# Performance work log

Measured on AMD Instinct MI355X. Metric: run time of the kernel, lower is better.

The kernel has to match this reference:

```python
import jax, jax.numpy as jnp
import numpy as np
import math

B, S, D, H = 16, 1024, 512, 8
DK = D // H  # 64
EPS_T = 1e-06   # temperature epsilon
LN_EPS = 1e-05  # torch LayerNorm default


def gelu_tanh(x):
    return 0.5 * x * (1 + jnp.tanh(math.sqrt(2.0 / math.pi) * (x + 0.044715 * x ** 3)))


def layer_norm(x, g, b):
    mu = jnp.mean(x, axis=-1, keepdims=True)
    var = jnp.mean((x - mu) ** 2, axis=-1, keepdims=True)
    return (x - mu) * jax.lax.rsqrt(var + LN_EPS) * g + b


def setup_inputs() -> dict:
    key = jax.random.key(0)
    ks = jax.random.split(key, 12)
    std_qkv = np.sqrt(2.0 / (D + D)).astype(np.float32)
    inp = {
        "Q": jax.random.normal(ks[0], (B, S, D), jnp.float32),
        "K": jax.random.normal(ks[1], (B, S, D), jnp.float32),
        "V": jax.random.normal(ks[2], (B, S, D), jnp.float32),
        "mask": jnp.zeros((B, S), dtype=bool),  # no padding
        "W_q": jax.random.normal(ks[3], (D, D), jnp.float32) * std_qkv,
        "W_k": jax.random.normal(ks[4], (D, D), jnp.float32) * std_qkv,
        "W_v": jax.random.normal(ks[5], (D, D), jnp.float32) * std_qkv,
        "W_o": jax.random.normal(ks[6], (D, D), jnp.float32) * std_qkv,
        "lin1_w": jax.random.normal(ks[7], (D, D), jnp.float32) * std_qkv,  # stored [in,out]
        "lin1_b": jnp.zeros((D,), jnp.float32),
        "lin2_w": jax.random.normal(ks[8], (D, D), jnp.float32) * std_qkv,
        "lin2_b": jnp.zeros((D,), jnp.float32),
        "ln_g": jnp.ones((D,), jnp.float32),
        "ln_b": jnp.zeros((D,), jnp.float32),
    }
    return inp


def reference(Q, K, V, mask, W_q, W_k, W_v, W_o, lin1_w, lin1_b, lin2_w, lin2_b, ln_g, ln_b):
    b, q_len, _ = Q.shape
    # projections -> (b, h, s, d_k)
    Qh = (Q @ W_q).reshape(b, q_len, H, DK).transpose(0, 2, 1, 3)
    Kh = (K @ W_k).reshape(b, q_len, H, DK).transpose(0, 2, 1, 3)
    Vh = (V @ W_v).reshape(b, q_len, H, DK).transpose(0, 2, 1, 3)

    temperature = DK ** 0.5
    scores = jnp.einsum("bhqd,bhkd->bhqk", Qh, Kh) / (temperature + EPS_T)

    # mask: causal triu(diag=1) OR pad mask broadcast along k (as in original)
    causal = jnp.triu(jnp.ones((q_len, q_len), dtype=bool), k=1)  # (q,k)
    pad = mask[:, None, :, None]                                  # (b,1,q,1)
    mask_ = causal[None, None, :, :] | pad                        # (b,1,q,k)
    scores = jnp.where(mask_, -1e10, scores)

    attn = jax.nn.softmax(scores, axis=-1)
    ctx = jnp.einsum("bhqk,bhkd->bhqd", attn, Vh)
    ctx = ctx.transpose(0, 2, 1, 3).reshape(b, q_len, H * DK)
    v_att = ctx @ W_o  # dropout = identity (eval)

    out = layer_norm(Q + v_att, ln_g, ln_b)
    ffn = gelu_tanh(out @ lin1_w + lin1_b) @ lin2_w + lin2_b
    out = layer_norm(ffn + out, ln_g, ln_b)
    return out
```

## Files before the change

### kernel.cpp

```cpp
#include <hip/hip_runtime.h>
#include <cstdint>

using f32x4  = __attribute__((ext_vector_type(4))) float;
using f16x8  = __attribute__((ext_vector_type(8))) _Float16;
using f16x4  = __attribute__((ext_vector_type(4))) _Float16;

#define DEV static __device__ __forceinline__

DEV _Float16 f2h(float f) { return (_Float16)f; }

DEV void gl2lds16(const void* g, void* l) {
  __builtin_amdgcn_global_load_lds(
      (__attribute__((address_space(1))) void*)(uintptr_t)g,
      (__attribute__((address_space(3))) void*)(uint32_t)(uintptr_t)l,
      16, 0, 0);
}

template <int MODE>
__global__ __launch_bounds__(256, 2) void gemm_k(
    const _Float16* __restrict__ A, const _Float16* __restrict__ Bt,
    const float* __restrict__ bias, float* __restrict__ outF,
    _Float16* __restrict__ outB) {
  __shared__ _Float16 As[128 * 32];
  __shared__ _Float16 Bs[128 * 32];
  const int tid = threadIdx.x;
  const int lane = tid & 63, wv = tid >> 6;
  const int quad = lane >> 4, l16 = lane & 15;
  const int wm = wv & 1, wn = wv >> 1;
  const int m0 = blockIdx.y * 128, n0 = blockIdx.x * 128;

  f32x4 acc[4][4] = {};

  const int c0 = tid, c1 = tid + 256;
  const int r0 = c0 >> 2, kp0 = c0 & 3, kl0 = kp0 ^ ((r0 >> 1) & 3);
  const int r1 = c1 >> 2, kp1 = c1 & 3, kl1 = kp1 ^ ((r1 >> 1) & 3);

  const _Float16* Ab = A + (size_t)m0 * 512;
  const _Float16* Bb = Bt + (size_t)n0 * 512;

  for (int kt = 0; kt < 512; kt += 32) {
    gl2lds16(Ab + (size_t)r0 * 512 + kt + kl0 * 8, &As[c0 * 8]);
    gl2lds16(Ab + (size_t)r1 * 512 + kt + kl1 * 8, &As[c1 * 8]);
    gl2lds16(Bb + (size_t)r0 * 512 + kt + kl0 * 8, &Bs[c0 * 8]);
    gl2lds16(Bb + (size_t)r1 * 512 + kt + kl1 * 8, &Bs[c1 * 8]);
    __syncthreads();
    f16x8 af[4], bfr[4];
#pragma unroll
    for (int i = 0; i < 4; i++) {
      int row = wm * 64 + i * 16 + l16;
      int q = quad ^ ((row >> 1) & 3);
      af[i] = *(const f16x8*)&As[row * 32 + q * 8];
    }
#pragma unroll
    for (int j = 0; j < 4; j++) {
      int row = wn * 64 + j * 16 + l16;
      int q = quad ^ ((row >> 1) & 3);
      bfr[j] = *(const f16x8*)&Bs[row * 32 + q * 8];
    }
#pragma unroll
    for (int i = 0; i < 4; i++)
#pragma unroll
      for (int j = 0; j < 4; j++)
        acc[i][j] = __builtin_amdgcn_mfma_f32_16x16x32_f16(af[i], bfr[j],
                                                           acc[i][j], 0, 0, 0);
    __syncthreads();
  }

#pragma unroll
  for (int i = 0; i < 4; i++) {
#pragma unroll
    for (int j = 0; j < 4; j++) {
      const size_t col = n0 + wn * 64 + j * 16 + l16;
#pragma unroll
      for (int r = 0; r < 4; r++) {
        const size_t row = m0 + wm * 64 + i * 16 + quad * 4 + r;
        float v = acc[i][j][r];
        if (MODE == 0) {
          size_t b = row >> 10, s = row & 1023, h = col >> 6, d = col & 63;
          outB[(((b * 8 + h) << 10) + s) * 64 + d] = f2h(v);
        } else if (MODE == 1) {
          outF[row * 512 + col] = v;
        } else if (MODE == 2) {
          float x = v + bias[col];
          float u = 0.7978845608028654f * (x + 0.044715f * x * x * x);
          float t = __expf(2.f * u);
          float th = 1.f - 2.f / (t + 1.f);
          outB[row * 512 + col] = f2h(0.5f * x * (1.f + th));
        } else {
          outF[row * 512 + col] = v + bias[col];
        }
      }
    }
  }
}

__global__ __launch_bounds__(256, 2) void attn_k(
    const _Float16* __restrict__ Qh, const _Float16* __restrict__ Kh,
    const _Float16* __restrict__ Vt, _Float16* __restrict__ ctx) {
  __shared__ _Float16 lds[16384];

  const int bid = blockIdx.x;
  const int qblk = 7 - (bid >> 7);
  const int bh = bid & 127;
  const int q0 = qblk * 128;
  const int ktmax = 2 * qblk + 1;

  const _Float16* Qp = Qh + (size_t)bh * 65536;
  const _Float16* Kp = Kh + (size_t)bh * 65536;
  const _Float16* Vp = Vt + (size_t)bh * 65536;

  const int tid = threadIdx.x, lane = tid & 63, wv = tid >> 6;
  const int quad = lane >> 4, l16 = lane & 15;
  const int s7 = l16 & 7;
  const int wdiag = 2 * qblk + (wv >> 1);

  f16x8 bq[2][2];
#pragma unroll
  for (int qs = 0; qs < 2; qs++)
#pragma unroll
    for (int kc = 0; kc < 2; kc++)
      bq[qs][kc] = *(const f16x8*)&Qp[(size_t)(q0 + wv * 32 + qs * 16 + l16) *
                                          64 +
                                      kc * 32 + quad * 8];
  int qg[2];
  qg[0] = q0 + wv * 32 + l16;
  qg[1] = qg[0] + 16;

  const float scale = 1.0f / (8.0f + 1e-6f);
  f32x4 ot[4][2] = {};
  float mrun[2] = {-3.0e38f, -3.0e38f};
  float lrun[2] = {0.f, 0.f};

  const int i0 = 2 * wv, i1 = 2 * wv + 1;
  const int lin0 = i0 * 64 + lane, lin1 = i1 * 64 + lane;
  const int rK0 = lin0 >> 3, chK0 = (lane & 7) ^ (rK0 & 7);
  const int rK1 = lin1 >> 3, chK1 = (lane & 7) ^ (rK1 & 7);

  auto stage = [&](int kt, int pb) {
    _Float16* Kb = lds + pb * 4096;
    _Float16* Vb = lds + 8192 + pb * 4096;
    gl2lds16(Kp + (size_t)(kt * 64 + rK0) * 64 + chK0 * 8, Kb + lin0 * 8);
    gl2lds16(Kp + (size_t)(kt * 64 + rK1) * 64 + chK1 * 8, Kb + lin1 * 8);
    gl2lds16(Vp + (size_t)rK0 * 1024 + kt * 64 + chK0 * 8, Vb + lin0 * 8);
    gl2lds16(Vp + (size_t)rK1 * 1024 + kt * 64 + chK1 * 8, Vb + lin1 * 8);
  };

  stage(0, 0);
  __syncthreads();

  for (int kt = 0; kt <= ktmax; kt++) {
    if (kt < ktmax) stage(kt + 1, (kt + 1) & 1);

    if (kt <= wdiag) {
      const _Float16* Ks = lds + (kt & 1) * 4096;
      const _Float16* Vs = lds + 8192 + (kt & 1) * 4096;

      f32x4 sa[4][2] = {};
#pragma unroll
      for (int ms = 0; ms < 4; ms++) {
        const int row = ms * 16 + l16;
        const int sl0 = quad ^ s7;
        f16x8 ka0 = *(const f16x8*)&Ks[row * 64 + sl0 * 8];
        f16x8 ka1 = *(const f16x8*)&Ks[row * 64 + (sl0 ^ 4) * 8];
#pragma unroll
        for (int qs = 0; qs < 2; qs++) {
          sa[ms][qs] = __builtin_amdgcn_mfma_f32_16x16x32_f16(
              ka0, bq[qs][0], sa[ms][qs], 0, 0, 0);
          sa[ms][qs] = __builtin_amdgcn_mfma_f32_16x16x32_f16(
              ka1, bq[qs][1], sa[ms][qs], 0, 0, 0);
        }
      }

      const bool diag = (kt == wdiag);
      float tmax[2] = {-3.0e38f, -3.0e38f};
#pragma unroll
      for (int ms = 0; ms < 4; ms++)
#pragma unroll
        for (int qs = 0; qs < 2; qs++)
#pragma unroll
          for (int r = 0; r < 4; r++) {
            float s = sa[ms][qs][r] * scale;
            if (diag) {
              int kg = kt * 64 + ms * 16 + quad * 4 + r;
              if (kg > qg[qs]) s = -3.0e38f;
            }
            sa[ms][qs][r] = s;
            tmax[qs] = fmaxf(tmax[qs], s);
          }

      float al[2];
#pragma unroll
      for (int qs = 0; qs < 2; qs++) {
        tmax[qs] = fmaxf(tmax[qs], __shfl_xor(tmax[qs], 16, 64));
        tmax[qs] = fmaxf(tmax[qs], __shfl_xor(tmax[qs], 32, 64));
        float mn = fmaxf(mrun[qs], tmax[qs]);
        al[qs] = __expf(mrun[qs] - mn);
        mrun[qs] = mn;
        lrun[qs] *= al[qs];
      }

      f16x4 pf[4][2];
#pragma unroll
      for (int ms = 0; ms < 4; ms++)
#pragma unroll
        for (int qs = 0; qs < 2; qs++) {
          f16x4 pk;
#pragma unroll
          for (int r = 0; r < 4; r++) {
            float p = __expf(sa[ms][qs][r] - mrun[qs]);
            lrun[qs] += p;
            pk[r] = f2h(p);
          }
          pf[ms][qs] = pk;
        }

#pragma unroll
      for (int ds = 0; ds < 4; ds++)
#pragma unroll
        for (int qs = 0; qs < 2; qs++)
#pragma unroll
          for (int r = 0; r < 4; r++) ot[ds][qs][r] *= al[qs];

#pragma unroll
      for (int ms = 0; ms < 4; ms++) {
        const int ch0 = (ms * 2 + (quad >> 1)) ^ s7;
#pragma unroll
        for (int ds = 0; ds < 4; ds++) {
          const int row = ds * 16 + l16;
          f16x4 vf =
              *(const f16x4*)&Vs[row * 64 + ch0 * 8 + (quad & 1) * 4];
#pragma unroll
          for (int qs = 0; qs < 2; qs++)
            ot[ds][qs] = __builtin_amdgcn_mfma_f32_16x16x16f16(
                vf, pf[ms][qs], ot[ds][qs], 0, 0, 0);
        }
      }
    }
    __syncthreads();
  }

  float rinv[2];
#pragma unroll
  for (int qs = 0; qs < 2; qs++) {
    lrun[qs] += __shfl_xor(lrun[qs], 16, 64);
    lrun[qs] += __shfl_xor(lrun[qs], 32, 64);
    rinv[qs] = 1.0f / lrun[qs];
  }

  _Float16* Ol = lds + wv * 2176;
#pragma unroll
  for (int ds = 0; ds < 4; ds++)
#pragma unroll
    for (int qs = 0; qs < 2; qs++) {
      f16x4 pk;
#pragma unroll
      for (int r = 0; r < 4; r++) pk[r] = f2h(ot[ds][qs][r] * rinv[qs]);
      *(f16x4*)&Ol[(qs * 16 + l16) * 68 + ds * 16 + quad * 4] = pk;
    }
  __syncthreads();

  const int b = bh >> 3, h = bh & 7;
#pragma unroll
  for (int rep = 0; rep < 4; rep++) {
    const int qq = rep * 8 + (lane >> 3);
    const int dc = lane & 7;
    f16x4 a = *(const f16x4*)&Ol[qq * 68 + dc * 8];
    f16x4 c = *(const f16x4*)&Ol[qq * 68 + dc * 8 + 4];
    f16x8 v;
    v[0] = a[0]; v[1] = a[1]; v[2] = a[2]; v[3] = a[3];
    v[4] = c[0]; v[5] = c[1]; v[6] = c[2]; v[7] = c[3];
    size_t row = (size_t)b * 1024 + q0 + wv * 32 + qq;
    *(f16x8*)&ctx[row * 512 + h * 64 + dc * 8] = v;
  }
}

__global__ void cast3_k(const float* __restrict__ Q, const float* __restrict__ K,
                        const float* __restrict__ V, _Float16* __restrict__ Qb,
                        _Float16* __restrict__ Kb, _Float16* __restrict__ Vb) {
  size_t i = (size_t)blockIdx.x * 256 + threadIdx.x;
  float4 q = ((const float4*)Q)[i];
  float4 k = ((const float4*)K)[i];
  float4 v = ((const float4*)V)[i];
  f16x4 o;
  o[0] = f2h(q.x); o[1] = f2h(q.y); o[2] = f2h(q.z); o[3] = f2h(q.w);
  ((f16x4*)Qb)[i] = o;
  o[0] = f2h(k.x); o[1] = f2h(k.y); o[2] = f2h(k.z); o[3] = f2h(k.w);
  ((f16x4*)Kb)[i] = o;
  o[0] = f2h(v.x); o[1] = f2h(v.y); o[2] = f2h(v.z); o[3] = f2h(v.w);
  ((f16x4*)Vb)[i] = o;
}

__global__ void wtrans_k(const float* W0, const float* W1, const float* W2,
                         const float* W3, const float* W4, const float* W5,
                         _Float16* dst) {
  __shared__ float t[32][33];
  const int z = blockIdx.z;
  const float* src = (z == 0) ? W0 : (z == 1) ? W1 : (z == 2) ? W2
                    : (z == 3) ? W3 : (z == 4) ? W4 : W5;
  _Float16* out = dst + (size_t)z * 262144;
  const int k0 = blockIdx.x * 32, n0 = blockIdx.y * 32;
  const int x = threadIdx.x, y = threadIdx.y;
  for (int j = y; j < 32; j += 8) t[j][x] = src[(size_t)(k0 + j) * 512 + n0 + x];
  __syncthreads();
  for (int j = y; j < 32; j += 8)
    out[(size_t)(n0 + j) * 512 + k0 + x] = f2h(t[x][j]);
}

__global__ void vtrans_k(const _Float16* __restrict__ Vh,
                         _Float16* __restrict__ Vt) {
  __shared__ _Float16 t[32][33];
  const int bh = blockIdx.z;
  const int s0 = blockIdx.x * 32, d0 = blockIdx.y * 32;
  const _Float16* src = Vh + (size_t)bh * 65536;
  _Float16* dst = Vt + (size_t)bh * 65536;
  const int x = threadIdx.x, y = threadIdx.y;
  for (int j = y; j < 32; j += 8) t[j][x] = src[(size_t)(s0 + j) * 64 + d0 + x];
  __syncthreads();
  for (int j = y; j < 32; j += 8)
    dst[(size_t)(d0 + j) * 1024 + s0 + x] = t[x][j];
}

template <bool WB>
__global__ __launch_bounds__(128) void ln_k(
    const float* __restrict__ X0, const float* __restrict__ X1,
    const float* __restrict__ g, const float* __restrict__ bb,
    float* __restrict__ outF, _Float16* __restrict__ outB) {
  __shared__ float sh[4];
  const int row = blockIdx.x, t = threadIdx.x;
  const size_t base = (size_t)row * 512 + t * 4;
  float4 a = *(const float4*)(X0 + base);
  float4 c = *(const float4*)(X1 + base);
  float x0 = a.x + c.x, x1 = a.y + c.y, x2 = a.z + c.z, x3 = a.w + c.w;
  float s = x0 + x1 + x2 + x3;
  float ss = x0 * x0 + x1 * x1 + x2 * x2 + x3 * x3;
#pragma unroll
  for (int off = 1; off <= 32; off <<= 1) {
    s += __shfl_xor(s, off, 64);
    ss += __shfl_xor(ss, off, 64);
  }
  if ((t & 63) == 0) { sh[(t >> 6) * 2] = s; sh[(t >> 6) * 2 + 1] = ss; }
  __syncthreads();
  s = sh[0] + sh[2];
  ss = sh[1] + sh[3];
  const float mu = s * (1.f / 512.f);
  const float var = ss * (1.f / 512.f) - mu * mu;
  const float rstd = rsqrtf(var + 1e-5f);
  float4 gv = *(const float4*)(g + t * 4);
  float4 bv = *(const float4*)(bb + t * 4);
  float y0 = (x0 - mu) * rstd * gv.x + bv.x;
  float y1 = (x1 - mu) * rstd * gv.y + bv.y;
  float y2 = (x2 - mu) * rstd * gv.z + bv.z;
  float y3 = (x3 - mu) * rstd * gv.w + bv.w;
  float4 o; o.x = y0; o.y = y1; o.z = y2; o.w = y3;
  *(float4*)(outF + base) = o;
  if (WB) {
    f16x4 ob; ob[0] = f2h(y0); ob[1] = f2h(y1); ob[2] = f2h(y2); ob[3] = f2h(y3);
    *(f16x4*)(outB + base) = ob;
  }
}

extern "C" void kernel_launch(void* const* d_in, const int* in_sizes, int n_in,
                              void* d_out, int out_size, void* d_ws,
                              size_t ws_size, hipStream_t stream) {
  const float* Q = (const float*)d_in[0];
  const float* K = (const float*)d_in[1];
  const float* V = (const float*)d_in[2];
  const float* Wq = (const float*)d_in[4];
  const float* Wk = (const float*)d_in[5];
  const float* Wv = (const float*)d_in[6];
  const float* Wo = (const float*)d_in[7];
  const float* l1w = (const float*)d_in[8];
  const float* l1b = (const float*)d_in[9];
  const float* l2w = (const float*)d_in[10];
  const float* l2b = (const float*)d_in[11];
  const float* lng = (const float*)d_in[12];
  const float* lnb = (const float*)d_in[13];
  float* out = (float*)d_out;

  uint8_t* w = (uint8_t*)d_ws;
  const size_t MB = 1ull << 20;
  _Float16* Qb = (_Float16*)(w + 0);
  _Float16* Kb = (_Float16*)(w + 16 * MB);
  _Float16* Vb = (_Float16*)(w + 32 * MB);
  _Float16* Wt = (_Float16*)(w + 48 * MB);
  _Float16* Qh = (_Float16*)(w + 52 * MB);
  _Float16* Kh = (_Float16*)(w + 68 * MB);
  _Float16* VhN = (_Float16*)(w + 84 * MB);
  _Float16* Vt = (_Float16*)(w + 100 * MB);
  float* vatt = (float*)(w + 100 * MB);
  float* f2 = (float*)(w + 100 * MB);
  float* out1f = (float*)(w + 132 * MB);
  _Float16* ctx = Qb;
  _Float16* h1 = Kb;
  _Float16* out1h = Vb;

  cast3_k<<<8192, 256, 0, stream>>>(Q, K, V, Qb, Kb, Vb);
  wtrans_k<<<dim3(16, 16, 6), dim3(32, 8), 0, stream>>>(Wq, Wk, Wv, Wo, l1w,
                                                        l2w, Wt);
  gemm_k<0><<<dim3(4, 128), 256, 0, stream>>>(Qb, Wt + 0 * 262144, nullptr,
                                              nullptr, Qh);
  gemm_k<0><<<dim3(4, 128), 256, 0, stream>>>(Kb, Wt + 1 * 262144, nullptr,
                                              nullptr, Kh);
  gemm_k<0><<<dim3(4, 128), 256, 0, stream>>>(Vb, Wt + 2 * 262144, nullptr,
                                              nullptr, VhN);
  vtrans_k<<<dim3(32, 2, 128), dim3(32, 8), 0, stream>>>(VhN, Vt);
  attn_k<<<1024, 256, 0, stream>>>(Qh, Kh, Vt, ctx);
  gemm_k<1><<<dim3(4, 128), 256, 0, stream>>>(ctx, Wt + 3 * 262144, nullptr,
                                              vatt, nullptr);
  ln_k<true><<<16384, 128, 0, stream>>>(Q, vatt, lng, lnb, out1f, out1h);
  gemm_k<2><<<dim3(4, 128), 256, 0, stream>>>(out1h, Wt + 4 * 262144, l1b,
                                              nullptr, h1);
  gemm_k<3><<<dim3(4, 128), 256, 0, stream>>>(h1, Wt + 5 * 262144, l2b, f2,
                                              nullptr);
  ln_k<false><<<16384, 128, 0, stream>>>(f2, out1f, lng, lnb, out, nullptr);
}
```

Before: 360.7 us.

## Batch QKV GEMMs, double-buffer GEMM K-tiles, pair attention blocks, fp16 intermediates

The QKV projections now run as one launch with a z-dimension. The GEMM uses double-buffered 64-wide K tiles, so loads overlap the MFMAs. Each attention block handles a balanced pair of causal query blocks, and the softmax uses exp2 with the scale folded into Q and packed fp16 row sums. The intermediates (attention output, residuals, FFN output) are stored as fp16 instead of fp32 to cut memory traffic. The layer norms read fp16 inputs and use the fp16 casts of Q and out1 as residuals, which lowers accuracy.

```diff
diff --git a/kernel.cpp b/kernel.cpp
--- a/kernel.cpp
+++ b/kernel.cpp
@@ -4,10 +4,17 @@
 using f32x4  = __attribute__((ext_vector_type(4))) float;
 using f16x8  = __attribute__((ext_vector_type(8))) _Float16;
 using f16x4  = __attribute__((ext_vector_type(4))) _Float16;
+using f16x2  = __attribute__((ext_vector_type(2))) _Float16;
 
 #define DEV static __device__ __forceinline__
 
 DEV _Float16 f2h(float f) { return (_Float16)f; }
+
+#if __has_builtin(__builtin_amdgcn_exp2f)
+#define EXP2(x) __builtin_amdgcn_exp2f(x)
+#else
+#define EXP2(x) __expf((x) * 0.6931471805599453f)
+#endif
 
 DEV void gl2lds16(const void* g, void* l) {
   __builtin_amdgcn_global_load_lds(
@@ -16,53 +23,79 @@
       16, 0, 0);
 }
 
+DEV f16x2 pack2(float a, float b) {
+  return __builtin_bit_cast(f16x2, __builtin_amdgcn_cvt_pkrtz(a, b));
+}
+
 template <int MODE>
 __global__ __launch_bounds__(256, 2) void gemm_k(
     const _Float16* __restrict__ A, const _Float16* __restrict__ Bt,
-    const float* __restrict__ bias, float* __restrict__ outF,
-    _Float16* __restrict__ outB) {
-  __shared__ _Float16 As[128 * 32];
-  __shared__ _Float16 Bs[128 * 32];
+    const float* __restrict__ bias, _Float16* __restrict__ outB) {
+  __shared__ _Float16 As[2][8192];
+  __shared__ _Float16 Bs[2][8192];
   const int tid = threadIdx.x;
   const int lane = tid & 63, wv = tid >> 6;
   const int quad = lane >> 4, l16 = lane & 15;
   const int wm = wv & 1, wn = wv >> 1;
   const int m0 = blockIdx.y * 128, n0 = blockIdx.x * 128;
 
+  const size_t zo = (MODE == 0) ? (size_t)blockIdx.z * 8388608 : 0;
+  const _Float16* Az = A + zo + (size_t)m0 * 512;
+  const _Float16* Bz = Bt + ((MODE == 0) ? (size_t)blockIdx.z * 262144 : 0) +
+                       (size_t)n0 * 512;
+  _Float16* Oz = outB + zo;
+
   f32x4 acc[4][4] = {};
 
-  const int c0 = tid, c1 = tid + 256;
-  const int r0 = c0 >> 2, kp0 = c0 & 3, kl0 = kp0 ^ ((r0 >> 1) & 3);
-  const int r1 = c1 >> 2, kp1 = c1 & 3, kl1 = kp1 ^ ((r1 >> 1) & 3);
-
-  const _Float16* Ab = A + (size_t)m0 * 512;
-  const _Float16* Bb = Bt + (size_t)n0 * 512;
-
-  for (int kt = 0; kt < 512; kt += 32) {
-    gl2lds16(Ab + (size_t)r0 * 512 + kt + kl0 * 8, &As[c0 * 8]);
-    gl2lds16(Ab + (size_t)r1 * 512 + kt + kl1 * 8, &As[c1 * 8]);
-    gl2lds16(Bb + (size_t)r0 * 512 + kt + kl0 * 8, &Bs[c0 * 8]);
-    gl2lds16(Bb + (size_t)r1 * 512 + kt + kl1 * 8, &Bs[c1 * 8]);
-    __syncthreads();
-    f16x8 af[4], bfr[4];
-#pragma unroll
-    for (int i = 0; i < 4; i++) {
-      int row = wm * 64 + i * 16 + l16;
-      int q = quad ^ ((row >> 1) & 3);
-      af[i] = *(const f16x8*)&As[row * 32 + q * 8];
+  int aoff[4];
+#pragma unroll
+  for (int j = 0; j < 4; j++) {
+    int e = j * 256 + tid;
+    int r = e >> 3, c = e & 7;
+    aoff[j] = r * 512 + (c ^ (r & 7)) * 8;
+  }
+
+  auto stage = [&](int kt, int pb) {
+    const _Float16* Ab = Az + kt * 64;
+    const _Float16* Bb = Bz + kt * 64;
+#pragma unroll
+    for (int j = 0; j < 4; j++)
+      gl2lds16(Ab + aoff[j], &As[pb][(j * 256 + tid) * 8]);
+#pragma unroll
+    for (int j = 0; j < 4; j++)
+      gl2lds16(Bb + aoff[j], &Bs[pb][(j * 256 + tid) * 8]);
+  };
+
+  stage(0, 0);
+  __syncthreads();
+
+  for (int kt = 0; kt < 8; kt++) {
+    const int pb = kt & 1;
+    if (kt < 7) stage(kt + 1, pb ^ 1);
+    f16x8 af[2][4], bf[2][4];
+#pragma unroll
+    for (int kc = 0; kc < 2; kc++) {
+#pragma unroll
+      for (int i = 0; i < 4; i++) {
+        int row = wm * 64 + i * 16 + l16;
+        int q = (kc * 4 + quad) ^ (row & 7);
+        af[kc][i] = *(const f16x8*)&As[pb][row * 64 + q * 8];
+      }
+#pragma unroll
+      for (int j = 0; j < 4; j++) {
+        int row = wn * 64 + j * 16 + l16;
+        int q = (kc * 4 + quad) ^ (row & 7);
+        bf[kc][j] = *(const f16x8*)&Bs[pb][row * 64 + q * 8];
+      }
     }
 #pragma unroll
-    for (int j = 0; j < 4; j++) {
-      int row = wn * 64 + j * 16 + l16;
-      int q = quad ^ ((row >> 1) & 3);
-      bfr[j] = *(const f16x8*)&Bs[row * 32 + q * 8];
-    }
-#pragma unroll
-    for (int i = 0; i < 4; i++)
-#pragma unroll
-      for (int j = 0; j < 4; j++)
-        acc[i][j] = __builtin_amdgcn_mfma_f32_16x16x32_f16(af[i], bfr[j],
-                                                           acc[i][j], 0, 0, 0);
+    for (int kc = 0; kc < 2; kc++)
+#pragma unroll
+      for (int i = 0; i < 4; i++)
+#pragma unroll
+        for (int j = 0; j < 4; j++)
+          acc[i][j] = __builtin_amdgcn_mfma_f32_16x16x32_f16(
+              af[kc][i], bf[kc][j], acc[i][j], 0, 0, 0);
     __syncthreads();
   }
 
@@ -77,17 +110,17 @@
         float v = acc[i][j][r];
         if (MODE == 0) {
           size_t b = row >> 10, s = row & 1023, h = col >> 6, d = col & 63;
-          outB[(((b * 8 + h) << 10) + s) * 64 + d] = f2h(v);
+          Oz[(((b * 8 + h) << 10) + s) * 64 + d] = f2h(v);
         } else if (MODE == 1) {
-          outF[row * 512 + col] = v;
+          Oz[row * 512 + col] = f2h(v);
         } else if (MODE == 2) {
           float x = v + bias[col];
           float u = 0.7978845608028654f * (x + 0.044715f * x * x * x);
           float t = __expf(2.f * u);
           float th = 1.f - 2.f / (t + 1.f);
-          outB[row * 512 + col] = f2h(0.5f * x * (1.f + th));
+          Oz[row * 512 + col] = f2h(0.5f * x * (1.f + th));
         } else {
-          outF[row * 512 + col] = v + bias[col];
+          Oz[row * 512 + col] = f2h(v + bias[col]);
         }
       }
     }
@@ -100,10 +133,8 @@
   __shared__ _Float16 lds[16384];
 
   const int bid = blockIdx.x;
-  const int qblk = 7 - (bid >> 7);
+  const int pair = bid >> 7;
   const int bh = bid & 127;
-  const int q0 = qblk * 128;
-  const int ktmax = 2 * qblk + 1;
 
   const _Float16* Qp = Qh + (size_t)bh * 65536;
   const _Float16* Kp = Kh + (size_t)bh * 65536;
@@ -112,27 +143,9 @@
   const int tid = threadIdx.x, lane = tid & 63, wv = tid >> 6;
   const int quad = lane >> 4, l16 = lane & 15;
   const int s7 = l16 & 7;
-  const int wdiag = 2 * qblk + (wv >> 1);
-
-  f16x8 bq[2][2];
-#pragma unroll
-  for (int qs = 0; qs < 2; qs++)
-#pragma unroll
-    for (int kc = 0; kc < 2; kc++)
-      bq[qs][kc] = *(const f16x8*)&Qp[(size_t)(q0 + wv * 32 + qs * 16 + l16) *
-                                          64 +
-                                      kc * 32 + quad * 8];
-  int qg[2];
-  qg[0] = q0 + wv * 32 + l16;
-  qg[1] = qg[0] + 16;
-
-  const float scale = 1.0f / (8.0f + 1e-6f);
-  f32x4 ot[4][2] = {};
-  float mrun[2] = {-3.0e38f, -3.0e38f};
-  float lrun[2] = {0.f, 0.f};
-
-  const int i0 = 2 * wv, i1 = 2 * wv + 1;
-  const int lin0 = i0 * 64 + lane, lin1 = i1 * 64 + lane;
+  const int b = bh >> 3, h = bh & 7;
+
+  const int lin0 = 2 * wv * 64 + lane, lin1 = (2 * wv + 1) * 64 + lane;
   const int rK0 = lin0 >> 3, chK0 = (lane & 7) ^ (rK0 & 7);
   const int rK1 = lin1 >> 3, chK1 = (lane & 7) ^ (rK1 & 7);
 
@@ -145,132 +158,169 @@
     gl2lds16(Vp + (size_t)rK1 * 1024 + kt * 64 + chK1 * 8, Vb + lin1 * 8);
   };
 
-  stage(0, 0);
-  __syncthreads();
-
-  for (int kt = 0; kt <= ktmax; kt++) {
-    if (kt < ktmax) stage(kt + 1, (kt + 1) & 1);
-
-    if (kt <= wdiag) {
-      const _Float16* Ks = lds + (kt & 1) * 4096;
-      const _Float16* Vs = lds + 8192 + (kt & 1) * 4096;
-
-      f32x4 sa[4][2] = {};
-#pragma unroll
-      for (int ms = 0; ms < 4; ms++) {
-        const int row = ms * 16 + l16;
-        const int sl0 = quad ^ s7;
-        f16x8 ka0 = *(const f16x8*)&Ks[row * 64 + sl0 * 8];
-        f16x8 ka1 = *(const f16x8*)&Ks[row * 64 + (sl0 ^ 4) * 8];
+  const _Float16 qsc = f2h((1.0f / (8.0f + 1e-6f)) * 1.4426950408889634f);
+  const f16x2 ones = {(_Float16)1.0f, (_Float16)1.0f};
+
+  for (int half = 0; half < 2; half++) {
+    const int qblk = half ? (7 - pair) : pair;
+    const int q0 = qblk * 128;
+    const int ktmax = 2 * qblk + 1;
+    const int wdiag = 2 * qblk + (wv >> 1);
+
+    f16x8 bq[2][2];
+#pragma unroll
+    for (int qs = 0; qs < 2; qs++)
+#pragma unroll
+      for (int kc = 0; kc < 2; kc++) {
+        f16x8 t = *(const f16x8*)&Qp[(size_t)(q0 + wv * 32 + qs * 16 + l16) *
+                                         64 +
+                                     kc * 32 + quad * 8];
+#pragma unroll
+        for (int r = 0; r < 8; r++) t[r] = t[r] * qsc;
+        bq[qs][kc] = t;
+      }
+    int qg[2];
+    qg[0] = q0 + wv * 32 + l16;
+    qg[1] = qg[0] + 16;
+
+    f32x4 ot[4][2] = {};
+    float mrun[2] = {-3.0e38f, -3.0e38f};
+    float lrun[2] = {0.f, 0.f};
+
+    stage(0, 0);
+    __syncthreads();
+
+    for (int kt = 0; kt <= ktmax; kt++) {
+      if (kt < ktmax) stage(kt + 1, (kt + 1) & 1);
+
+      if (kt <= wdiag) {
+        const _Float16* Ks = lds + (kt & 1) * 4096;
+        const _Float16* Vs = lds + 8192 + (kt & 1) * 4096;
+
+        f32x4 sa[4][2] = {};
+#pragma unroll
+        for (int ms = 0; ms < 4; ms++) {
+          const int row = ms * 16 + l16;
+          const int sl0 = quad ^ s7;
+          f16x8 ka0 = *(const f16x8*)&Ks[row * 64 + sl0 * 8];
+          f16x8 ka1 = *(const f16x8*)&Ks[row * 64 + (sl0 ^ 4) * 8];
+#pragma unroll
+          for (int qs = 0; qs < 2; qs++) {
+            sa[ms][qs] = __builtin_amdgcn_mfma_f32_16x16x32_f16(
+                ka0, bq[qs][0], sa[ms][qs], 0, 0, 0);
+            sa[ms][qs] = __builtin_amdgcn_mfma_f32_16x16x32_f16(
+                ka1, bq[qs][1], sa[ms][qs], 0, 0, 0);
+          }
+        }
+
+        if (kt == wdiag) {
+#pragma unroll
+          for (int ms = 0; ms < 4; ms++)
+#pragma unroll
+            for (int qs = 0; qs < 2; qs++)
+#pragma unroll
+              for (int r = 0; r < 4; r++) {
+                int kg = kt * 64 + ms * 16 + quad * 4 + r;
+                if (kg > qg[qs]) sa[ms][qs][r] = -3.0e38f;
+              }
+        }
+
+        float tmax[2] = {-3.0e38f, -3.0e38f};
+#pragma unroll
+        for (int ms = 0; ms < 4; ms++)
+#pragma unroll
+          for (int qs = 0; qs < 2; qs++)
+#pragma unroll
+            for (int r = 0; r < 4; r++)
+              tmax[qs] = fmaxf(tmax[qs], sa[ms][qs][r]);
+
+        float al[2];
 #pragma unroll
         for (int qs = 0; qs < 2; qs++) {
-          sa[ms][qs] = __builtin_amdgcn_mfma_f32_16x16x32_f16(
-              ka0, bq[qs][0], sa[ms][qs], 0, 0, 0);
-          sa[ms][qs] = __builtin_amdgcn_mfma_f32_16x16x32_f16(
-              ka1, bq[qs][1], sa[ms][qs], 0, 0, 0);
+          tmax[qs] = fmaxf(tmax[qs], __shfl_xor(tmax[qs], 16, 64));
+          tmax[qs] = fmaxf(tmax[qs], __shfl_xor(tmax[qs], 32, 64));
+          float mn = fmaxf(mrun[qs], tmax[qs]);
+          al[qs] = EXP2(mrun[qs] - mn);
+          mrun[qs] = mn;
+          lrun[qs] *= al[qs];
         }
-      }
-
-      const bool diag = (kt == wdiag);
-      float tmax[2] = {-3.0e38f, -3.0e38f};
-#pragma unroll
-      for (int ms = 0; ms < 4; ms++)
-#pragma unroll
-        for (int qs = 0; qs < 2; qs++)
-#pragma unroll
-          for (int r = 0; r < 4; r++) {
-            float s = sa[ms][qs][r] * scale;
-            if (diag) {
-              int kg = kt * 64 + ms * 16 + quad * 4 + r;
-              if (kg > qg[qs]) s = -3.0e38f;
-            }
-            sa[ms][qs][r] = s;
-            tmax[qs] = fmaxf(tmax[qs], s);
+
+        f16x4 pf[4][2];
+#pragma unroll
+        for (int ms = 0; ms < 4; ms++)
+#pragma unroll
+          for (int qs = 0; qs < 2; qs++) {
+            float e0 = EXP2(sa[ms][qs][0] - mrun[qs]);
+            float e1 = EXP2(sa[ms][qs][1] - mrun[qs]);
+            float e2 = EXP2(sa[ms][qs][2] - mrun[qs]);
+            float e3 = EXP2(sa[ms][qs][3] - mrun[qs]);
+            f16x2 lo = pack2(e0, e1);
+            f16x2 hi = pack2(e2, e3);
+            lrun[qs] = __builtin_amdgcn_fdot2(lo, ones, lrun[qs], false);
+            lrun[qs] = __builtin_amdgcn_fdot2(hi, ones, lrun[qs], false);
+            f16x4 pk;
+            pk[0] = lo[0]; pk[1] = lo[1]; pk[2] = hi[0]; pk[3] = hi[1];
+            pf[ms][qs] = pk;
           }
 
-      float al[2];
+#pragma unroll
+        for (int ds = 0; ds < 4; ds++)
+#pragma unroll
+          for (int qs = 0; qs < 2; qs++)
+#pragma unroll
+            for (int r = 0; r < 4; r++) ot[ds][qs][r] *= al[qs];
+
+#pragma unroll
+        for (int ms = 0; ms < 4; ms++) {
+          const int ch0 = (ms * 2 + (quad >> 1)) ^ s7;
+#pragma unroll
+          for (int ds = 0; ds < 4; ds++) {
+            const int row = ds * 16 + l16;
+            f16x4 vf =
+                *(const f16x4*)&Vs[row * 64 + ch0 * 8 + (quad & 1) * 4];
+#pragma unroll
+            for (int qs = 0; qs < 2; qs++)
+              ot[ds][qs] = __builtin_amdgcn_mfma_f32_16x16x16f16(
+                  vf, pf[ms][qs], ot[ds][qs], 0, 0, 0);
+          }
+        }
+      }
+      __syncthreads();
+    }
+
+    float rinv[2];
+#pragma unroll
+    for (int qs = 0; qs < 2; qs++) {
+      lrun[qs] += __shfl_xor(lrun[qs], 16, 64);
+      lrun[qs] += __shfl_xor(lrun[qs], 32, 64);
+      rinv[qs] = 1.0f / lrun[qs];
+    }
+
+    _Float16* Ol = lds + wv * 2176;
+#pragma unroll
+    for (int ds = 0; ds < 4; ds++)
 #pragma unroll
       for (int qs = 0; qs < 2; qs++) {
-        tmax[qs] = fmaxf(tmax[qs], __shfl_xor(tmax[qs], 16, 64));
-        tmax[qs] = fmaxf(tmax[qs], __shfl_xor(tmax[qs], 32, 64));
-        float mn = fmaxf(mrun[qs], tmax[qs]);
-        al[qs] = __expf(mrun[qs] - mn);
-        mrun[qs] = mn;
-        lrun[qs] *= al[qs];
-      }
-
-      f16x4 pf[4][2];
-#pragma unroll
-      for (int ms = 0; ms < 4; ms++)
-#pragma unroll
-        for (int qs = 0; qs < 2; qs++) {
-          f16x4 pk;
-#pragma unroll
-          for (int r = 0; r < 4; r++) {
-            float p = __expf(sa[ms][qs][r] - mrun[qs]);
-            lrun[qs] += p;
-            pk[r] = f2h(p);
-          }
-          pf[ms][qs] = pk;
-        }
-
-#pragma unroll
-      for (int ds = 0; ds < 4; ds++)
-#pragma unroll
-        for (int qs = 0; qs < 2; qs++)
-#pragma unroll
-          for (int r = 0; r < 4; r++) ot[ds][qs][r] *= al[qs];
-
-#pragma unroll
-      for (int ms = 0; ms < 4; ms++) {
-        const int ch0 = (ms * 2 + (quad >> 1)) ^ s7;
-#pragma unroll
-        for (int ds = 0; ds < 4; ds++) {
-          const int row = ds * 16 + l16;
-          f16x4 vf =
-              *(const f16x4*)&Vs[row * 64 + ch0 * 8 + (quad & 1) * 4];
-#pragma unroll
-          for (int qs = 0; qs < 2; qs++)
-            ot[ds][qs] = __builtin_amdgcn_mfma_f32_16x16x16f16(
-                vf, pf[ms][qs], ot[ds][qs], 0, 0, 0);
-        }
-      }
+        f16x4 pk;
+#pragma unroll
+        for (int r = 0; r < 4; r++) pk[r] = f2h(ot[ds][qs][r] * rinv[qs]);
+        *(f16x4*)&Ol[(qs * 16 + l16) * 68 + ds * 16 + quad * 4] = pk;
+      }
+    __syncthreads();
+
+#pragma unroll
+    for (int rep = 0; rep < 4; rep++) {
+      const int qq = rep * 8 + (lane >> 3);
+      const int dc = lane & 7;
+      f16x4 a = *(const f16x4*)&Ol[qq * 68 + dc * 8];
+      f16x4 c = *(const f16x4*)&Ol[qq * 68 + dc * 8 + 4];
+      f16x8 v;
+      v[0] = a[0]; v[1] = a[1]; v[2] = a[2]; v[3] = a[3];
+      v[4] = c[0]; v[5] = c[1]; v[6] = c[2]; v[7] = c[3];
+      size_t row = (size_t)b * 1024 + q0 + wv * 32 + qq;
+      *(f16x8*)&ctx[row * 512 + h * 64 + dc * 8] = v;
     }
     __syncthreads();
-  }
-
-  float rinv[2];
-#pragma unroll
-  for (int qs = 0; qs < 2; qs++) {
-    lrun[qs] += __shfl_xor(lrun[qs], 16, 64);
-    lrun[qs] += __shfl_xor(lrun[qs], 32, 64);
-    rinv[qs] = 1.0f / lrun[qs];
-  }
-
-  _Float16* Ol = lds + wv * 2176;
-#pragma unroll
-  for (int ds = 0; ds < 4; ds++)
-#pragma unroll
-    for (int qs = 0; qs < 2; qs++) {
-      f16x4 pk;
-#pragma unroll
-      for (int r = 0; r < 4; r++) pk[r] = f2h(ot[ds][qs][r] * rinv[qs]);
-      *(f16x4*)&Ol[(qs * 16 + l16) * 68 + ds * 16 + quad * 4] = pk;
-    }
-  __syncthreads();
-
-  const int b = bh >> 3, h = bh & 7;
-#pragma unroll
-  for (int rep = 0; rep < 4; rep++) {
-    const int qq = rep * 8 + (lane >> 3);
-    const int dc = lane & 7;
-    f16x4 a = *(const f16x4*)&Ol[qq * 68 + dc * 8];
-    f16x4 c = *(const f16x4*)&Ol[qq * 68 + dc * 8 + 4];
-    f16x8 v;
-    v[0] = a[0]; v[1] = a[1]; v[2] = a[2]; v[3] = a[3];
-    v[4] = c[0]; v[5] = c[1]; v[6] = c[2]; v[7] = c[3];
-    size_t row = (size_t)b * 1024 + q0 + wv * 32 + qq;
-    *(f16x8*)&ctx[row * 512 + h * 64 + dc * 8] = v;
   }
 }
 
@@ -320,17 +370,20 @@
     dst[(size_t)(d0 + j) * 1024 + s0 + x] = t[x][j];
 }
 
-template <bool WB>
+template <bool F32OUT>
 __global__ __launch_bounds__(128) void ln_k(
-    const float* __restrict__ X0, const float* __restrict__ X1,
+    const _Float16* __restrict__ X0, const _Float16* __restrict__ X1,
     const float* __restrict__ g, const float* __restrict__ bb,
     float* __restrict__ outF, _Float16* __restrict__ outB) {
   __shared__ float sh[4];
   const int row = blockIdx.x, t = threadIdx.x;
-  const size_t base = (size_t)row * 512 + t * 4;
-  float4 a = *(const float4*)(X0 + base);
-  float4 c = *(const float4*)(X1 + base);
-  float x0 = a.x + c.x, x1 = a.y + c.y, x2 = a.z + c.z, x3 = a.w + c.w;
+  const size_t base4 = (size_t)row * 128 + t;
+  f16x4 a = ((const f16x4*)X0)[base4];
+  f16x4 c = ((const f16x4*)X1)[base4];
+  float x0 = (float)a[0] + (float)c[0];
+  float x1 = (float)a[1] + (float)c[1];
+  float x2 = (float)a[2] + (float)c[2];
+  float x3 = (float)a[3] + (float)c[3];
   float s = x0 + x1 + x2 + x3;
   float ss = x0 * x0 + x1 * x1 + x2 * x2 + x3 * x3;
 #pragma unroll
@@ -351,11 +404,12 @@
   float y1 = (x1 - mu) * rstd * gv.y + bv.y;
   float y2 = (x2 - mu) * rstd * gv.z + bv.z;
   float y3 = (x3 - mu) * rstd * gv.w + bv.w;
-  float4 o; o.x = y0; o.y = y1; o.z = y2; o.w = y3;
-  *(float4*)(outF + base) = o;
-  if (WB) {
+  if (F32OUT) {
+    float4 o; o.x = y0; o.y = y1; o.z = y2; o.w = y3;
+    *(float4*)(outF + (size_t)row * 512 + t * 4) = o;
+  } else {
     f16x4 ob; ob[0] = f2h(y0); ob[1] = f2h(y1); ob[2] = f2h(y2); ob[3] = f2h(y3);
-    *(f16x4*)(outB + base) = ob;
+    ((f16x4*)outB)[base4] = ob;
   }
 }
 
@@ -387,30 +441,22 @@
   _Float16* Kh = (_Float16*)(w + 68 * MB);
   _Float16* VhN = (_Float16*)(w + 84 * MB);
   _Float16* Vt = (_Float16*)(w + 100 * MB);
-  float* vatt = (float*)(w + 100 * MB);
-  float* f2 = (float*)(w + 100 * MB);
-  float* out1f = (float*)(w + 132 * MB);
-  _Float16* ctx = Qb;
+  _Float16* ctx = VhN;
+  _Float16* vatt = Vt;
   _Float16* h1 = Kb;
   _Float16* out1h = Vb;
+  _Float16* f2b = Qh;
 
   cast3_k<<<8192, 256, 0, stream>>>(Q, K, V, Qb, Kb, Vb);
   wtrans_k<<<dim3(16, 16, 6), dim3(32, 8), 0, stream>>>(Wq, Wk, Wv, Wo, l1w,
                                                         l2w, Wt);
-  gemm_k<0><<<dim3(4, 128), 256, 0, stream>>>(Qb, Wt + 0 * 262144, nullptr,
-                                              nullptr, Qh);
-  gemm_k<0><<<dim3(4, 128), 256, 0, stream>>>(Kb, Wt + 1 * 262144, nullptr,
-                                              nullptr, Kh);
-  gemm_k<0><<<dim3(4, 128), 256, 0, stream>>>(Vb, Wt + 2 * 262144, nullptr,
-                                              nullptr, VhN);
+  gemm_k<0><<<dim3(4, 128, 3), 256, 0, stream>>>(Qb, Wt, nullptr, Qh);
   vtrans_k<<<dim3(32, 2, 128), dim3(32, 8), 0, stream>>>(VhN, Vt);
-  attn_k<<<1024, 256, 0, stream>>>(Qh, Kh, Vt, ctx);
+  attn_k<<<512, 256, 0, stream>>>(Qh, Kh, Vt, ctx);
   gemm_k<1><<<dim3(4, 128), 256, 0, stream>>>(ctx, Wt + 3 * 262144, nullptr,
-                                              vatt, nullptr);
-  ln_k<true><<<16384, 128, 0, stream>>>(Q, vatt, lng, lnb, out1f, out1h);
-  gemm_k<2><<<dim3(4, 128), 256, 0, stream>>>(out1h, Wt + 4 * 262144, l1b,
-                                              nullptr, h1);
-  gemm_k<3><<<dim3(4, 128), 256, 0, stream>>>(h1, Wt + 5 * 262144, l2b, f2,
-                                              nullptr);
-  ln_k<false><<<16384, 128, 0, stream>>>(f2, out1f, lng, lnb, out, nullptr);
-}
+                                              vatt);
+  ln_k<false><<<16384, 128, 0, stream>>>(Qb, vatt, lng, lnb, nullptr, out1h);
+  gemm_k<2><<<dim3(4, 128), 256, 0, stream>>>(out1h, Wt + 4 * 262144, l1b, h1);
+  gemm_k<3><<<dim3(4, 128), 256, 0, stream>>>(h1, Wt + 5 * 262144, l2b, f2b);
+  ln_k<true><<<16384, 128, 0, stream>>>(f2b, out1h, lng, lnb, out, nullptr);
+}
```

New measurement: 317.5 us. -12.0%, faster.
